# Optimization experiments

Measured on AMD Instinct MI355X. Metric: run time of the kernel, lower is better.

The kernel has to match this reference:

```python
import jax, jax.numpy as jnp
import numpy as np
from jax import lax

EPS = 1e-06


def _ema_scan(x, s):
    # x: [B, C, T]; s: [C] smoothing coeff in [0, 1]
    # Recurrence: y_0 = x_0; y_t = s * x_t + (1 - s) * y_{t-1}
    # Expressed as affine pairs (A_t, b_t) with y_t = A_t * y_{t-1} + b_t
    s_b = s[None, :, None]  # [1, C, 1]
    A0 = jnp.zeros_like(x[:, :, :1])
    A_rest = jnp.broadcast_to(1.0 - s_b, x[:, :, 1:].shape)
    A = jnp.concatenate([A0, A_rest], axis=2)
    b = jnp.concatenate([x[:, :, :1], s_b * x[:, :, 1:]], axis=2)

    def combine(c1, c2):
        a1, b1 = c1
        a2, b2 = c2
        return (a1 * a2, a2 * b1 + b2)

    _, ema = lax.associative_scan(combine, (A, b), axis=2)
    return ema


def setup_inputs() -> dict:
    key = jax.random.key(0)
    B, C, T = 32, 128, 16000
    kx, = jax.random.split(key, 1)
    x = jax.random.uniform(kx, (B, C, T), dtype=jnp.float32)
    alpha = jnp.ones((C,), dtype=jnp.float32) * 0.96
    delta = jnp.ones((C,), dtype=jnp.float32) * 2.0
    root = jnp.ones((C,), dtype=jnp.float32) * 2.0
    ema_weights = jnp.ones((C,), dtype=jnp.float32) * 0.04
    return {"x": x, "alpha": alpha, "delta": delta, "root": root, "ema_weights": ema_weights}


def reference(x, alpha, delta, root, ema_weights):
    # sPCEN: per-channel EMA smoother + power-law compression
    s = jnp.clip(ema_weights, 0.0, 1.0)
    ema = _ema_scan(x, s)  # [B, C, T]

    alpha_c = jnp.minimum(alpha, 1.0)[None, :, None]
    root_c = jnp.maximum(root, 1.0)[None, :, None]
    r = 1.0 / root_c
    d = delta[None, :, None]

    out = (x / (EPS + ema) ** alpha_c + d) ** r - d ** r
    return out
```

## Files before the change

kernel.cpp:

```cpp
#include <hip/hip_runtime.h>
#include <math.h>

#define T_LEN    16000
#define T_LEN4   4000
#define THREADS  256
#define CHUNK    17
#define TILE     (THREADS * CHUNK)
#define TILE4    (TILE / 4)
#define NT       4
#define EPS_F    1e-6f

__launch_bounds__(THREADS, 4)
__global__ void pcen_kernel(const float* __restrict__ x,
                            const float* __restrict__ alpha,
                            const float* __restrict__ delta,
                            const float* __restrict__ root,
                            const float* __restrict__ ema_w,
                            float* __restrict__ out, int C) {
    __shared__ __align__(16) float buf[2][TILE];
    __shared__ float swA[4], swB[4];

    const int row  = blockIdx.x;
    const int c    = row % C;
    const int tid  = threadIdx.x;
    const int lane = tid & 63;
    const int wave = tid >> 6;

    const float s   = fminf(fmaxf(ema_w[c], 0.0f), 1.0f);
    const float q   = 1.0f - s;
    const float a_c = fminf(alpha[c], 1.0f);
    const float r   = 1.0f / fmaxf(root[c], 1.0f);
    const float d   = delta[c];
    const float dr  = powf(d, r);
    const float q17 = powf(q, (float)CHUNK);
    const bool  sqrt_path = (r == 0.5f);

    const float4* x4 = (const float4*)(x   + (size_t)row * T_LEN);
    float4*       o4 = (float4*)      (out + (size_t)row * T_LEN);

    const int lbase = tid * CHUNK;
    float e_carry = 0.0f;

    float4 g0, g1, g2, g3, g4 = make_float4(1.f, 1.f, 1.f, 1.f);

    auto load_tile = [&](int t) {
        const int b = t * TILE4;
        g0 = (b + tid        < T_LEN4) ? x4[b + tid       ] : make_float4(1.f,1.f,1.f,1.f);
        g1 = (b + tid +  256 < T_LEN4) ? x4[b + tid +  256] : make_float4(1.f,1.f,1.f,1.f);
        g2 = (b + tid +  512 < T_LEN4) ? x4[b + tid +  512] : make_float4(1.f,1.f,1.f,1.f);
        g3 = (b + tid +  768 < T_LEN4) ? x4[b + tid +  768] : make_float4(1.f,1.f,1.f,1.f);
        if (tid < TILE4 - 1024)
            g4 = (b + tid + 1024 < T_LEN4) ? x4[b + tid + 1024] : make_float4(1.f,1.f,1.f,1.f);
    };

    load_tile(0);

    for (int t = 0; t < NT; ++t) {
        float*  cb  = &buf[t & 1][0];
        float4* cb4 = (float4*)cb;

        cb4[tid]       = g0;
        cb4[tid + 256] = g1;
        cb4[tid + 512] = g2;
        cb4[tid + 768] = g3;
        if (tid < TILE4 - 1024) cb4[tid + 1024] = g4;
        __syncthreads();

        if (t + 1 < NT) load_tile(t + 1);

        float xv[CHUNK];
        #pragma unroll
        for (int j = 0; j < CHUNK; ++j) xv[j] = cb[lbase + j];

        const bool ft = (t == 0) && (tid == 0);
        float la = ft ? 0.0f   : q17;
        float lb = ft ? xv[0]  : s * xv[0];
        #pragma unroll
        for (int j = 1; j < CHUNK; ++j) lb = fmaf(q, lb, s * xv[j]);

        #pragma unroll
        for (int off = 1; off < 64; off <<= 1) {
            float ua = __shfl_up(la, off);
            float ub = __shfl_up(lb, off);
            if (lane >= off) { lb = fmaf(la, ub, lb); la *= ua; }
        }
        if (lane == 63) { swA[wave] = la; swB[wave] = lb; }
        __syncthreads();

        float pa = 1.0f, pb = 0.0f;
        #pragma unroll
        for (int w = 0; w < 3; ++w)
            if (w < wave) { pb = fmaf(swA[w], pb, swB[w]); pa *= swA[w]; }

        float ea = __shfl_up(la, 1);
        float eb = __shfl_up(lb, 1);
        float a_ex, b_ex;
        if (lane == 0) { a_ex = pa;      b_ex = pb; }
        else           { a_ex = pa * ea; b_ex = fmaf(ea, pb, eb); }
        float e = fmaf(a_ex, e_carry, b_ex);

        float ta = 1.0f, tb = 0.0f;
        #pragma unroll
        for (int w = 0; w < 4; ++w) { tb = fmaf(swA[w], tb, swB[w]); ta *= swA[w]; }
        e_carry = fmaf(ta, e_carry, tb);

        if (t * TILE + lbase < T_LEN) {
            if (sqrt_path) {
                #pragma unroll
                for (int j = 0; j < CHUNK; ++j) {
                    float xvj = xv[j];
                    e = (ft && j == 0) ? xvj : fmaf(q, e, s * xvj);
                    float lge = log2f(EPS_F + e);
                    float v   = xvj * exp2f(-a_c * lge);
                    cb[lbase + j] = sqrtf(v + d) - dr;
                }
            } else {
                #pragma unroll
                for (int j = 0; j < CHUNK; ++j) {
                    float xvj = xv[j];
                    e = (ft && j == 0) ? xvj : fmaf(q, e, s * xvj);
                    float lge = log2f(EPS_F + e);
                    float v   = xvj * exp2f(-a_c * lge);
                    cb[lbase + j] = exp2f(r * log2f(v + d)) - dr;
                }
            }
        }
        __syncthreads();

        {
            const int b = t * TILE4;
            if (b + tid        < T_LEN4) o4[b + tid       ] = cb4[tid];
            if (b + tid +  256 < T_LEN4) o4[b + tid +  256] = cb4[tid + 256];
            if (b + tid +  512 < T_LEN4) o4[b + tid +  512] = cb4[tid + 512];
            if (b + tid +  768 < T_LEN4) o4[b + tid +  768] = cb4[tid + 768];
            if (tid < TILE4 - 1024 && b + tid + 1024 < T_LEN4)
                o4[b + tid + 1024] = cb4[tid + 1024];
        }
    }
}

extern "C" void kernel_launch(void* const* d_in, const int* in_sizes, int n_in,
                              void* d_out, int out_size, void* d_ws, size_t ws_size,
                              hipStream_t stream) {
    const float* x     = (const float*)d_in[0];
    const float* alpha = (const float*)d_in[1];
    const float* delta = (const float*)d_in[2];
    const float* root  = (const float*)d_in[3];
    const float* ema_w = (const float*)d_in[4];
    float* out = (float*)d_out;

    const int C    = in_sizes[1];
    const int rows = in_sizes[0] / T_LEN;

    pcen_kernel<<<rows, THREADS, 0, stream>>>(x, alpha, delta, root, ema_w, out, C);
}
```

Baseline: 447.6 us.

## Load chunks directly into registers, dropping the shared-memory staging tile

Each thread now reads its 16 contiguous samples straight from global memory as four float4 loads and writes results back the same way. This removes the shared-memory transpose buffer and two block barriers per tile. The chunk size changes from 17 to 16 so that 4 tiles of 4096 cover the 16000 samples, and the occupancy hint rises to 6 blocks. The trade-off is that per-thread global accesses are now strided across lanes (each lane reads 64 contiguous bytes), so coalescing is worse, and the software prefetch of the next tile is gone.

```diff
diff --git a/kernel.cpp b/kernel.cpp
--- a/kernel.cpp
+++ b/kernel.cpp
@@ -4,21 +4,19 @@
 #define T_LEN    16000
 #define T_LEN4   4000
 #define THREADS  256
-#define CHUNK    17
-#define TILE     (THREADS * CHUNK)
-#define TILE4    (TILE / 4)
+#define CHUNK    16
+#define TILE4    (THREADS * 4)
 #define NT       4
 #define EPS_F    1e-6f
 
-__launch_bounds__(THREADS, 4)
+__launch_bounds__(THREADS, 6)
 __global__ void pcen_kernel(const float* __restrict__ x,
                             const float* __restrict__ alpha,
                             const float* __restrict__ delta,
                             const float* __restrict__ root,
                             const float* __restrict__ ema_w,
                             float* __restrict__ out, int C) {
-    __shared__ __align__(16) float buf[2][TILE];
-    __shared__ float swA[4], swB[4];
+    __shared__ float swA[2][4], swB[2][4];
 
     const int row  = blockIdx.x;
     const int c    = row % C;
@@ -32,49 +30,32 @@
     const float r   = 1.0f / fmaxf(root[c], 1.0f);
     const float d   = delta[c];
     const float dr  = powf(d, r);
-    const float q17 = powf(q, (float)CHUNK);
+    const float q16 = powf(q, (float)CHUNK);
     const bool  sqrt_path = (r == 0.5f);
 
     const float4* x4 = (const float4*)(x   + (size_t)row * T_LEN);
     float4*       o4 = (float4*)      (out + (size_t)row * T_LEN);
 
-    const int lbase = tid * CHUNK;
     float e_carry = 0.0f;
 
-    float4 g0, g1, g2, g3, g4 = make_float4(1.f, 1.f, 1.f, 1.f);
+    for (int t = 0; t < NT; ++t) {
+        const int  base4 = t * TILE4 + tid * 4;
+        const bool valid = (base4 < T_LEN4);
+        const int  p     = t & 1;
 
-    auto load_tile = [&](int t) {
-        const int b = t * TILE4;
-        g0 = (b + tid        < T_LEN4) ? x4[b + tid       ] : make_float4(1.f,1.f,1.f,1.f);
-        g1 = (b + tid +  256 < T_LEN4) ? x4[b + tid +  256] : make_float4(1.f,1.f,1.f,1.f);
-        g2 = (b + tid +  512 < T_LEN4) ? x4[b + tid +  512] : make_float4(1.f,1.f,1.f,1.f);
-        g3 = (b + tid +  768 < T_LEN4) ? x4[b + tid +  768] : make_float4(1.f,1.f,1.f,1.f);
-        if (tid < TILE4 - 1024)
-            g4 = (b + tid + 1024 < T_LEN4) ? x4[b + tid + 1024] : make_float4(1.f,1.f,1.f,1.f);
-    };
-
-    load_tile(0);
-
-    for (int t = 0; t < NT; ++t) {
-        float*  cb  = &buf[t & 1][0];
-        float4* cb4 = (float4*)cb;
-
-        cb4[tid]       = g0;
-        cb4[tid + 256] = g1;
-        cb4[tid + 512] = g2;
-        cb4[tid + 768] = g3;
-        if (tid < TILE4 - 1024) cb4[tid + 1024] = g4;
-        __syncthreads();
-
-        if (t + 1 < NT) load_tile(t + 1);
-
-        float xv[CHUNK];
-        #pragma unroll
-        for (int j = 0; j < CHUNK; ++j) xv[j] = cb[lbase + j];
+        float4 v0, v1, v2, v3;
+        if (valid) {
+            v0 = x4[base4 + 0]; v1 = x4[base4 + 1];
+            v2 = x4[base4 + 2]; v3 = x4[base4 + 3];
+        } else {
+            v0 = v1 = v2 = v3 = make_float4(1.f, 1.f, 1.f, 1.f);
+        }
+        float xv[CHUNK] = { v0.x, v0.y, v0.z, v0.w,  v1.x, v1.y, v1.z, v1.w,
+                            v2.x, v2.y, v2.z, v2.w,  v3.x, v3.y, v3.z, v3.w };
 
         const bool ft = (t == 0) && (tid == 0);
-        float la = ft ? 0.0f   : q17;
-        float lb = ft ? xv[0]  : s * xv[0];
+        float la = ft ? 0.0f  : q16;
+        float lb = ft ? xv[0] : s * xv[0];
         #pragma unroll
         for (int j = 1; j < CHUNK; ++j) lb = fmaf(q, lb, s * xv[j]);
 
@@ -84,13 +65,13 @@
             float ub = __shfl_up(lb, off);
             if (lane >= off) { lb = fmaf(la, ub, lb); la *= ua; }
         }
-        if (lane == 63) { swA[wave] = la; swB[wave] = lb; }
+        if (lane == 63) { swA[p][wave] = la; swB[p][wave] = lb; }
         __syncthreads();
 
         float pa = 1.0f, pb = 0.0f;
         #pragma unroll
         for (int w = 0; w < 3; ++w)
-            if (w < wave) { pb = fmaf(swA[w], pb, swB[w]); pa *= swA[w]; }
+            if (w < wave) { pb = fmaf(swA[p][w], pb, swB[p][w]); pa *= swA[p][w]; }
 
         float ea = __shfl_up(la, 1);
         float eb = __shfl_up(lb, 1);
@@ -101,10 +82,10 @@
 
         float ta = 1.0f, tb = 0.0f;
         #pragma unroll
-        for (int w = 0; w < 4; ++w) { tb = fmaf(swA[w], tb, swB[w]); ta *= swA[w]; }
+        for (int w = 0; w < 4; ++w) { tb = fmaf(swA[p][w], tb, swB[p][w]); ta *= swA[p][w]; }
         e_carry = fmaf(ta, e_carry, tb);
 
-        if (t * TILE + lbase < T_LEN) {
+        if (valid) {
             if (sqrt_path) {
                 #pragma unroll
                 for (int j = 0; j < CHUNK; ++j) {
@@ -112,7 +93,7 @@
                     e = (ft && j == 0) ? xvj : fmaf(q, e, s * xvj);
                     float lge = log2f(EPS_F + e);
                     float v   = xvj * exp2f(-a_c * lge);
-                    cb[lbase + j] = sqrtf(v + d) - dr;
+                    xv[j] = sqrtf(v + d) - dr;
                 }
             } else {
                 #pragma unroll
@@ -121,20 +102,13 @@
                     e = (ft && j == 0) ? xvj : fmaf(q, e, s * xvj);
                     float lge = log2f(EPS_F + e);
                     float v   = xvj * exp2f(-a_c * lge);
-                    cb[lbase + j] = exp2f(r * log2f(v + d)) - dr;
+                    xv[j] = exp2f(r * log2f(v + d)) - dr;
                 }
             }
-        }
-        __syncthreads();
-
-        {
-            const int b = t * TILE4;
-            if (b + tid        < T_LEN4) o4[b + tid       ] = cb4[tid];
-            if (b + tid +  256 < T_LEN4) o4[b + tid +  256] = cb4[tid + 256];
-            if (b + tid +  512 < T_LEN4) o4[b + tid +  512] = cb4[tid + 512];
-            if (b + tid +  768 < T_LEN4) o4[b + tid +  768] = cb4[tid + 768];
-            if (tid < TILE4 - 1024 && b + tid + 1024 < T_LEN4)
-                o4[b + tid + 1024] = cb4[tid + 1024];
+            o4[base4 + 0] = make_float4(xv[ 0], xv[ 1], xv[ 2], xv[ 3]);
+            o4[base4 + 1] = make_float4(xv[ 4], xv[ 5], xv[ 6], xv[ 7]);
+            o4[base4 + 2] = make_float4(xv[ 8], xv[ 9], xv[10], xv[11]);
+            o4[base4 + 3] = make_float4(xv[12], xv[13], xv[14], xv[15]);
         }
     }
 }
```

After: 456.0 us. Within noise of the previous version (+1.9%).
